# Kernel optimization log

Measured on AMD Instinct MI355X. Metric: run time of the kernel, lower is better.

Reference implementation:

```python
import jax, jax.numpy as jnp
import numpy as np

N = 100000      # num nodes (in_features)
E = 1600000     # num edges
P = 100000      # num pos/neg label edges
EMB = 64        # embedding dim (hardcoded 64 in Encoder)
HID = 128       # 2 * out_channels
OUT = 64        # out_channels
EPS = 1e-15     # PyG GAE EPS
MAX_LOGSTD = 10.0


def setup_inputs() -> dict:
    key = jax.random.key(0)
    ks = jax.random.split(key, 10)
    emb_weight = jax.random.normal(ks[0], (N, EMB), dtype=jnp.float32) * 0.1
    edge_index = jax.random.randint(ks[1], (2, E), 0, N, dtype=jnp.int64)
    pos_edge_label_index = jax.random.randint(ks[2], (2, P), 0, N, dtype=jnp.int64)
    neg_edge_label_index = jax.random.randint(ks[3], (2, P), 0, N, dtype=jnp.int64)
    W1 = jax.random.normal(ks[4], (EMB, HID), dtype=jnp.float32) / np.sqrt(EMB)
    b1 = jnp.zeros((HID,), dtype=jnp.float32)
    W_mu = jax.random.normal(ks[5], (HID, OUT), dtype=jnp.float32) / np.sqrt(HID)
    b_mu = jnp.zeros((OUT,), dtype=jnp.float32)
    W_ls = jax.random.normal(ks[6], (HID, OUT), dtype=jnp.float32) / np.sqrt(HID)
    b_ls = jnp.zeros((OUT,), dtype=jnp.float32)
    return {
        'emb_weight': emb_weight, 'edge_index': edge_index,
        'W1': W1, 'b1': b1, 'W_mu': W_mu, 'b_mu': b_mu, 'W_ls': W_ls, 'b_ls': b_ls,
        'pos_edge_label_index': pos_edge_label_index,
        'neg_edge_label_index': neg_edge_label_index,
    }


def gcn_conv(x, src, dst, deg_inv_sqrt, W, b):
    # GCNConv with added self-loops and symmetric normalization:
    # out = D^{-1/2} (A + I) D^{-1/2} (x W) + b
    h = x @ W                                  # [N, F_out]
    norm = deg_inv_sqrt[src] * deg_inv_sqrt[dst]          # [E]
    agg = jax.ops.segment_sum(h[src] * norm[:, None], dst, num_segments=N)
    agg = agg + h * (deg_inv_sqrt * deg_inv_sqrt)[:, None]  # self-loop term
    return agg + b


def reference(emb_weight, edge_index, W1, b1, W_mu, b_mu, W_ls, b_ls,
              pos_edge_label_index, neg_edge_label_index):
    src, dst = edge_index[0], edge_index[1]
    # degree includes self-loop weight 1
    deg = jax.ops.segment_sum(jnp.ones((E,), dtype=emb_weight.dtype), dst, num_segments=N) + 1.0
    deg_inv_sqrt = jax.lax.rsqrt(deg)

    h = jax.nn.relu(gcn_conv(emb_weight, src, dst, deg_inv_sqrt, W1, b1))
    mu = gcn_conv(h, src, dst, deg_inv_sqrt, W_mu, b_mu)
    logstd = jnp.minimum(gcn_conv(h, src, dst, deg_inv_sqrt, W_ls, b_ls), MAX_LOGSTD)
    z = mu  # eval-mode reparametrize returns mu

    # recon_loss: inner-product decoder + BCE on pos/neg label edges
    ps, pd = pos_edge_label_index[0], pos_edge_label_index[1]
    ns, nd = neg_edge_label_index[0], neg_edge_label_index[1]
    pos_p = jax.nn.sigmoid(jnp.sum(z[ps] * z[pd], axis=-1))
    neg_p = jax.nn.sigmoid(jnp.sum(z[ns] * z[nd], axis=-1))
    pos_loss = -jnp.mean(jnp.log(pos_p + EPS))
    neg_loss = -jnp.mean(jnp.log(1.0 - neg_p + EPS))
    loss = pos_loss + neg_loss
    return z, logstd, loss
```

## Files before the change

kernel.cpp:

```cpp
#include <hip/hip_runtime.h>
#include <hip/hip_bf16.h>
#include <hip/hip_fp16.h>

#define NN 100000
#define NE 1600000
#define NP 100000

typedef _Float16 h2v __attribute__((ext_vector_type(2)));

__device__ __forceinline__ float fdot2u(uint a, uint b, float c) {
    union { uint u; h2v h; } ua, ub;
    ua.u = a; ub.u = b;
    return __builtin_amdgcn_fdot2(ua.h, ub.h, c, false);
}

__device__ __forceinline__ uint packh2(float lo, float hi) {
    __half2 h = __floats2half2_rn(lo, hi);
    return *(uint*)&h;
}

__device__ __forceinline__ void h8_to_f(const uint4 u, float* f) {
    const __half2* hp = (const __half2*)&u;
    float2 t0 = __half22float2(hp[0]), t1 = __half22float2(hp[1]);
    float2 t2 = __half22float2(hp[2]), t3 = __half22float2(hp[3]);
    f[0] = t0.x; f[1] = t0.y; f[2] = t1.x; f[3] = t1.y;
    f[4] = t2.x; f[5] = t2.y; f[6] = t3.x; f[7] = t3.y;
}

__device__ __forceinline__ void add8(const uint4 u, float* acc) {
    float f[8]; h8_to_f(u, f);
#pragma unroll
    for (int i = 0; i < 8; ++i) acc[i] += f[i];
}

__device__ __forceinline__ uint4 f_to_h8(const float* f) {
    union { __half2 h[4]; uint4 u; } pk;
    pk.h[0] = __floats2half2_rn(f[0], f[1]);
    pk.h[1] = __floats2half2_rn(f[2], f[3]);
    pk.h[2] = __floats2half2_rn(f[4], f[5]);
    pk.h[3] = __floats2half2_rn(f[6], f[7]);
    return pk.u;
}

#define RNG 400
#define NBK 250
#define K_A 8000
#define CAPB 12288

__global__ __launch_bounds__(256) void k_hist(const int* __restrict__ ei,
                                              int* __restrict__ bcnt) {
    __shared__ int hist[NBK];
    int tid = threadIdx.x;
    int e0 = blockIdx.x * K_A;
    for (int i = tid; i < NBK; i += 256) hist[i] = 0;
    __syncthreads();
    for (int i = tid; i < K_A; i += 256) atomicAdd(&hist[ei[NE + e0 + i] / RNG], 1);
    __syncthreads();
    for (int i = tid; i < NBK; i += 256) if (hist[i]) atomicAdd(&bcnt[i], hist[i]);
}

__global__ __launch_bounds__(256) void k_bscan(const int* __restrict__ bcnt,
                                               int* __restrict__ bbase,
                                               int* __restrict__ gcnt) {
    __shared__ int c[NBK];
    int tid = threadIdx.x;
    if (tid < NBK) c[tid] = bcnt[tid];
    __syncthreads();
    if (tid < 64) {
        int run = 0;
        for (int g = 0; g < NBK; g += 64) {
            int idx = g + tid;
            int v = (idx < NBK) ? c[idx] : 0;
            int inc = v;
#pragma unroll
            for (int off = 1; off < 64; off <<= 1) {
                int t2 = __shfl_up(inc, off);
                if (tid >= off) inc += t2;
            }
            if (idx < NBK) { int ex = run + inc - v; bbase[idx] = ex; gcnt[idx] = ex; }
            run += __shfl(inc, 63);
        }
        if (tid == 0) bbase[NBK] = run;
    }
}

__global__ __launch_bounds__(256) void k_binA(const int* __restrict__ ei,
                                              int* __restrict__ gcnt,
                                              int* __restrict__ edges) {
    __shared__ int buf[K_A];
    __shared__ int hist[NBK], lofs[NBK + 1], lcnt[NBK], gbase[NBK];
    int tid = threadIdx.x;
    int e0 = blockIdx.x * K_A;
    for (int i = tid; i < NBK; i += 256) { hist[i] = 0; lcnt[i] = 0; }
    __syncthreads();
    for (int i = tid; i < K_A; i += 256) atomicAdd(&hist[ei[NE + e0 + i] / RNG], 1);
    __syncthreads();
    if (tid < 64) {
        int run = 0;
        for (int g = 0; g < NBK; g += 64) {
            int idx = g + tid;
            int v = (idx < NBK) ? hist[idx] : 0;
            int inc = v;
#pragma unroll
            for (int off = 1; off < 64; off <<= 1) {
                int t2 = __shfl_up(inc, off);
                if (tid >= off) inc += t2;
            }
            if (idx < NBK) lofs[idx] = run + inc - v;
            run += __shfl(inc, 63);
        }
        if (tid == 0) lofs[NBK] = run;
    }
    for (int i = tid; i < NBK; i += 256) gbase[i] = atomicAdd(&gcnt[i], hist[i]);
    __syncthreads();
    for (int i = tid; i < K_A; i += 256) {
        int s = ei[e0 + i], d = ei[NE + e0 + i];
        int b = d / RNG;
        int dl = d - b * RNG;
        int p = lofs[b] + atomicAdd(&lcnt[b], 1);
        buf[p] = s | (dl << 17);
    }
    __syncthreads();
    for (int j = tid; j < K_A; j += 256) {
        int loB = 0, hiB = NBK;
        while (hiB - loB > 1) {
            int mid = (loB + hiB) >> 1;
            if (lofs[mid] <= j) loB = mid; else hiB = mid;
        }
        edges[gbase[loB] + (j - lofs[loB])] = buf[j];
    }
}

__global__ __launch_bounds__(256) void k_binB(const int* __restrict__ bbase,
                                              int* __restrict__ edges,
                                              int* __restrict__ rowptr,
                                              float* __restrict__ dinv) {
    __shared__ int buf[CAPB];
    __shared__ int hist[RNG], lrp[RNG], lcnt[RNG];
    int tid = threadIdx.x;
    int b = blockIdx.x;
    int lo = b * RNG;
    int base = bbase[b], n = bbase[b + 1] - base;
    for (int i = tid; i < RNG; i += 256) { hist[i] = 0; lcnt[i] = 0; }
    __syncthreads();
    for (int i = tid; i < n; i += 256)
        atomicAdd(&hist[((unsigned)edges[base + i]) >> 17], 1);
    __syncthreads();
    if (tid < 64) {
        int run = 0;
        for (int g = 0; g < RNG; g += 64) {
            int idx = g + tid;
            int v = (idx < RNG) ? hist[idx] : 0;
            int inc = v;
#pragma unroll
            for (int off = 1; off < 64; off <<= 1) {
                int t2 = __shfl_up(inc, off);
                if (tid >= off) inc += t2;
            }
            if (idx < RNG) lrp[idx] = run + inc - v;
            run += __shfl(inc, 63);
        }
    }
    __syncthreads();
    for (int i = tid; i < RNG; i += 256) {
        dinv[lo + i] = rsqrtf((float)hist[i] + 1.0f);
        rowptr[lo + i] = base + lrp[i];
    }
    if (b == NBK - 1 && tid == 0) rowptr[NN] = base + n;
    int ovS0 = -1, ovS1 = -1, ovR0 = 0, ovR1 = 0;
    for (int i = tid; i < n; i += 256) {
        int rec = edges[base + i];
        int dl = ((unsigned)rec) >> 17;
        int src = rec & 0x1FFFF;
        int slot = lrp[dl] + atomicAdd(&lcnt[dl], 1);
        if (slot < CAPB) buf[slot] = src;
        else if (ovS0 < 0) { ovS0 = slot; ovR0 = src; }
        else { ovS1 = slot; ovR1 = src; }
    }
    __syncthreads();
    int lim = n < CAPB ? n : CAPB;
    for (int i = tid; i < lim; i += 256) edges[base + i] = buf[i];
    if (ovS0 >= 0) edges[base + ovS0] = ovR0;
    if (ovS1 >= 0) edges[base + ovS1] = ovR1;
}

__global__ void k_cvt(const float4* __restrict__ in4, const float* __restrict__ dinv,
                      uint4* __restrict__ out) {
    int t = blockIdx.x * blockDim.x + threadIdx.x;
    if (t >= NN * 8) return;
    float dv = dinv[t >> 3];
    float4 a = in4[t * 2], b = in4[t * 2 + 1];
    float f[8] = {a.x * dv, a.y * dv, a.z * dv, a.w * dv,
                  b.x * dv, b.y * dv, b.z * dv, b.w * dv};
    out[t] = f_to_h8(f);
}

__global__ __launch_bounds__(256) void k_aggE(const uint4* __restrict__ x16,
                                              const float* __restrict__ dinv,
                                              const int* __restrict__ rowptr,
                                              const int* __restrict__ edges,
                                              uint4* __restrict__ aggE16) {
    int t = blockIdx.x * blockDim.x + threadIdx.x;
    int r = t >> 3, q = t & 7;
    float dr = dinv[r];
    float acc[8];
    h8_to_f(x16[(size_t)r * 8 + q], acc);
    int j = rowptr[r], j1 = rowptr[r + 1];
    for (; j + 8 <= j1; j += 8) {
        int e[8]; uint4 v[8];
#pragma unroll
        for (int i = 0; i < 8; ++i) e[i] = edges[j + i];
#pragma unroll
        for (int i = 0; i < 8; ++i) v[i] = x16[(size_t)e[i] * 8 + q];
#pragma unroll
        for (int i = 0; i < 8; ++i) add8(v[i], acc);
    }
    if (j + 4 <= j1) {
        int e[4]; uint4 v[4];
#pragma unroll
        for (int i = 0; i < 4; ++i) e[i] = edges[j + i];
#pragma unroll
        for (int i = 0; i < 4; ++i) v[i] = x16[(size_t)e[i] * 8 + q];
#pragma unroll
        for (int i = 0; i < 4; ++i) add8(v[i], acc);
        j += 4;
    }
    for (; j < j1; ++j) add8(x16[(size_t)edges[j] * 8 + q], acc);
    float o[8];
#pragma unroll
    for (int i = 0; i < 8; ++i) o[i] = acc[i] * dr;
    aggE16[(size_t)r * 8 + q] = f_to_h8(o);
}

__global__ __launch_bounds__(256) void k_aggH(const uint4* __restrict__ x16,
                                              const float* __restrict__ dinv,
                                              const int* __restrict__ rowptr,
                                              const int* __restrict__ edges,
                                              uint4* __restrict__ aggH16) {
    int t = blockIdx.x * blockDim.x + threadIdx.x;
    int r = t >> 4, q = t & 15;
    float dr = dinv[r];
    float acc[8];
    h8_to_f(x16[(size_t)r * 16 + q], acc);
    int j = rowptr[r], j1 = rowptr[r + 1];
    for (; j + 8 <= j1; j += 8) {
        int e[8]; uint4 v[8];
#pragma unroll
        for (int i = 0; i < 8; ++i) e[i] = edges[j + i];
#pragma unroll
        for (int i = 0; i < 8; ++i) v[i] = x16[(size_t)e[i] * 16 + q];
#pragma unroll
        for (int i = 0; i < 8; ++i) add8(v[i], acc);
    }
    if (j + 4 <= j1) {
        int e[4]; uint4 v[4];
#pragma unroll
        for (int i = 0; i < 4; ++i) e[i] = edges[j + i];
#pragma unroll
        for (int i = 0; i < 4; ++i) v[i] = x16[(size_t)e[i] * 16 + q];
#pragma unroll
        for (int i = 0; i < 4; ++i) add8(v[i], acc);
        j += 4;
    }
    for (; j < j1; ++j) add8(x16[(size_t)edges[j] * 16 + q], acc);
    float o[8];
#pragma unroll
    for (int i = 0; i < 8; ++i) o[i] = acc[i] * dr;
    aggH16[(size_t)r * 16 + q] = f_to_h8(o);
}

__global__ __launch_bounds__(256) void k_h(const uint4* __restrict__ aggE16,
                                           const float4* __restrict__ W1_4,
                                           const float* __restrict__ b1,
                                           const float* __restrict__ dinv,
                                           uint2* __restrict__ h16) {
    __shared__ uint4 w16h[32 * 32];
    __shared__ uint rows16[32 * 32];
    __shared__ float sdinv[32];
    int t = threadIdx.x;
    int base = blockIdx.x * 32;
#pragma unroll
    for (int i = 0; i < 4; ++i) {
        int idx = t + i * 256;
        int kp = idx >> 5, jg = idx & 31;
        float4 we = W1_4[(2 * kp) * 32 + jg];
        float4 wo = W1_4[(2 * kp + 1) * 32 + jg];
        w16h[idx] = make_uint4(packh2(we.x, wo.x), packh2(we.y, wo.y),
                               packh2(we.z, wo.z), packh2(we.w, wo.w));
    }
    {
        int r = t >> 3, c = t & 7;
        ((uint4*)rows16)[r * 8 + c] = aggE16[(size_t)(base + r) * 8 + c];
    }
    if (t < 32) sdinv[t] = dinv[base + t];
    __syncthreads();
    int rg = t >> 5, jg = t & 31;
    int r0 = rg * 4;
    float4 bias = ((const float4*)b1)[jg];
    float acc[4][4];
#pragma unroll
    for (int r = 0; r < 4; ++r) {
        acc[r][0] = bias.x; acc[r][1] = bias.y; acc[r][2] = bias.z; acc[r][3] = bias.w;
    }
#pragma unroll 4
    for (int kp = 0; kp < 32; ++kp) {
        uint f0 = rows16[(r0 + 0) * 32 + kp];
        uint f1 = rows16[(r0 + 1) * 32 + kp];
        uint f2 = rows16[(r0 + 2) * 32 + kp];
        uint f3 = rows16[(r0 + 3) * 32 + kp];
        uint4 wv = w16h[kp * 32 + jg];
        acc[0][0] = fdot2u(f0, wv.x, acc[0][0]); acc[0][1] = fdot2u(f0, wv.y, acc[0][1]);
        acc[0][2] = fdot2u(f0, wv.z, acc[0][2]); acc[0][3] = fdot2u(f0, wv.w, acc[0][3]);
        acc[1][0] = fdot2u(f1, wv.x, acc[1][0]); acc[1][1] = fdot2u(f1, wv.y, acc[1][1]);
        acc[1][2] = fdot2u(f1, wv.z, acc[1][2]); acc[1][3] = fdot2u(f1, wv.w, acc[1][3]);
        acc[2][0] = fdot2u(f2, wv.x, acc[2][0]); acc[2][1] = fdot2u(f2, wv.y, acc[2][1]);
        acc[2][2] = fdot2u(f2, wv.z, acc[2][2]); acc[2][3] = fdot2u(f2, wv.w, acc[2][3]);
        acc[3][0] = fdot2u(f3, wv.x, acc[3][0]); acc[3][1] = fdot2u(f3, wv.y, acc[3][1]);
        acc[3][2] = fdot2u(f3, wv.z, acc[3][2]); acc[3][3] = fdot2u(f3, wv.w, acc[3][3]);
    }
#pragma unroll
    for (int r = 0; r < 4; ++r) {
        float dv = sdinv[r0 + r];
        union { __half2 h[2]; uint2 u; } pk;
        pk.h[0] = __floats2half2_rn(fmaxf(acc[r][0], 0.0f) * dv, fmaxf(acc[r][1], 0.0f) * dv);
        pk.h[1] = __floats2half2_rn(fmaxf(acc[r][2], 0.0f) * dv, fmaxf(acc[r][3], 0.0f) * dv);
        h16[(size_t)(base + r0 + r) * 32 + jg] = pk.u;
    }
}

__global__ __launch_bounds__(256) void k_out(const uint4* __restrict__ aggH16,
                                             const float4* __restrict__ Wmu4,
                                             const float* __restrict__ bmu,
                                             const float4* __restrict__ Wls4,
                                             const float* __restrict__ bls,
                                             float* __restrict__ out,
                                             uint2* __restrict__ z16) {
    __shared__ uint4 w16h[64 * 32];
    __shared__ uint rows16[32 * 64];
    int t = threadIdx.x;
    int base = blockIdx.x * 32;
#pragma unroll
    for (int i = 0; i < 8; ++i) {
        int idx = t + i * 256;
        int kp = idx >> 5, jg = idx & 31;
        int jj = (jg < 16) ? jg : (jg - 16);
        const float4* W = (jg < 16) ? Wmu4 : Wls4;
        float4 we = W[(2 * kp) * 16 + jj];
        float4 wo = W[(2 * kp + 1) * 16 + jj];
        w16h[idx] = make_uint4(packh2(we.x, wo.x), packh2(we.y, wo.y),
                               packh2(we.z, wo.z), packh2(we.w, wo.w));
    }
#pragma unroll
    for (int i = 0; i < 2; ++i) {
        int idx = t + i * 256;
        int r = idx >> 4, c = idx & 15;
        ((uint4*)rows16)[r * 16 + c] = aggH16[(size_t)(base + r) * 16 + c];
    }
    __syncthreads();
    int rg = t >> 5, jg = t & 31;
    int r0 = rg * 4;
    float4 bias = (jg < 16) ? ((const float4*)bmu)[jg] : ((const float4*)bls)[jg - 16];
    float acc[4][4];
#pragma unroll
    for (int r = 0; r < 4; ++r) {
        acc[r][0] = bias.x; acc[r][1] = bias.y; acc[r][2] = bias.z; acc[r][3] = bias.w;
    }
#pragma unroll 4
    for (int kp = 0; kp < 64; ++kp) {
        uint f0 = rows16[(r0 + 0) * 64 + kp];
        uint f1 = rows16[(r0 + 1) * 64 + kp];
        uint f2 = rows16[(r0 + 2) * 64 + kp];
        uint f3 = rows16[(r0 + 3) * 64 + kp];
        uint4 wv = w16h[kp * 32 + jg];
        acc[0][0] = fdot2u(f0, wv.x, acc[0][0]); acc[0][1] = fdot2u(f0, wv.y, acc[0][1]);
        acc[0][2] = fdot2u(f0, wv.z, acc[0][2]); acc[0][3] = fdot2u(f0, wv.w, acc[0][3]);
        acc[1][0] = fdot2u(f1, wv.x, acc[1][0]); acc[1][1] = fdot2u(f1, wv.y, acc[1][1]);
        acc[1][2] = fdot2u(f1, wv.z, acc[1][2]); acc[1][3] = fdot2u(f1, wv.w, acc[1][3]);
        acc[2][0] = fdot2u(f2, wv.x, acc[2][0]); acc[2][1] = fdot2u(f2, wv.y, acc[2][1]);
        acc[2][2] = fdot2u(f2, wv.z, acc[2][2]); acc[2][3] = fdot2u(f2, wv.w, acc[2][3]);
        acc[3][0] = fdot2u(f3, wv.x, acc[3][0]); acc[3][1] = fdot2u(f3, wv.y, acc[3][1]);
        acc[3][2] = fdot2u(f3, wv.z, acc[3][2]); acc[3][3] = fdot2u(f3, wv.w, acc[3][3]);
    }
    float4* out4 = (float4*)out;
    if (jg < 16) {
#pragma unroll
        for (int r = 0; r < 4; ++r) {
            out4[(size_t)(base + r0 + r) * 16 + jg] =
                make_float4(acc[r][0], acc[r][1], acc[r][2], acc[r][3]);
            union { __half2 h[2]; uint2 u; } pk;
            pk.h[0] = __floats2half2_rn(acc[r][0], acc[r][1]);
            pk.h[1] = __floats2half2_rn(acc[r][2], acc[r][3]);
            z16[(size_t)(base + r0 + r) * 16 + jg] = pk.u;
        }
    } else {
#pragma unroll
        for (int r = 0; r < 4; ++r) {
            float4 o = make_float4(fminf(acc[r][0], 10.0f), fminf(acc[r][1], 10.0f),
                                   fminf(acc[r][2], 10.0f), fminf(acc[r][3], 10.0f));
            out4[(size_t)NN * 16 + (size_t)(base + r0 + r) * 16 + (jg - 16)] = o;
        }
    }
}

__global__ __launch_bounds__(256) void k_loss(const int* __restrict__ pos,
                                              const int* __restrict__ neg,
                                              const uint2* __restrict__ z16,
                                              float* __restrict__ accum) {
    int t = blockIdx.x * blockDim.x + threadIdx.x;
    int grp = t >> 4, q = t & 15;
    int e0 = grp * 4;
    bool isNeg = e0 >= NP;
    const int* idx = isNeg ? neg : pos;
    int eb = isNeg ? e0 - NP : e0;
    int a0 = idx[eb + 0], b0 = idx[NP + eb + 0];
    int a1 = idx[eb + 1], b1 = idx[NP + eb + 1];
    int a2 = idx[eb + 2], b2 = idx[NP + eb + 2];
    int a3 = idx[eb + 3], b3 = idx[NP + eb + 3];
    uint2 ua0 = z16[(size_t)a0 * 16 + q], ub0 = z16[(size_t)b0 * 16 + q];
    uint2 ua1 = z16[(size_t)a1 * 16 + q], ub1 = z16[(size_t)b1 * 16 + q];
    uint2 ua2 = z16[(size_t)a2 * 16 + q], ub2 = z16[(size_t)b2 * 16 + q];
    uint2 ua3 = z16[(size_t)a3 * 16 + q], ub3 = z16[(size_t)b3 * 16 + q];
    float d0 = fdot2u(ua0.y, ub0.y, fdot2u(ua0.x, ub0.x, 0.0f));
    float d1 = fdot2u(ua1.y, ub1.y, fdot2u(ua1.x, ub1.x, 0.0f));
    float d2 = fdot2u(ua2.y, ub2.y, fdot2u(ua2.x, ub2.x, 0.0f));
    float d3 = fdot2u(ua3.y, ub3.y, fdot2u(ua3.x, ub3.x, 0.0f));
#pragma unroll
    for (int off = 1; off < 16; off <<= 1) {
        d0 += __shfl_xor(d0, off);
        d1 += __shfl_xor(d1, off);
        d2 += __shfl_xor(d2, off);
        d3 += __shfl_xor(d3, off);
    }
    __shared__ float bsum[2];
    if (threadIdx.x < 2) bsum[threadIdx.x] = 0.0f;
    __syncthreads();
    if (q == 0) {
        float term;
        if (isNeg) {
            term = logf(1.0f - 1.0f / (1.0f + expf(-d0)) + 1e-15f)
                 + logf(1.0f - 1.0f / (1.0f + expf(-d1)) + 1e-15f)
                 + logf(1.0f - 1.0f / (1.0f + expf(-d2)) + 1e-15f)
                 + logf(1.0f - 1.0f / (1.0f + expf(-d3)) + 1e-15f);
        } else {
            term = logf(1.0f / (1.0f + expf(-d0)) + 1e-15f)
                 + logf(1.0f / (1.0f + expf(-d1)) + 1e-15f)
                 + logf(1.0f / (1.0f + expf(-d2)) + 1e-15f)
                 + logf(1.0f / (1.0f + expf(-d3)) + 1e-15f);
        }
        atomicAdd(&bsum[isNeg ? 1 : 0], term);
    }
    __syncthreads();
    if (threadIdx.x < 2) atomicAdd(&accum[threadIdx.x], bsum[threadIdx.x]);
}

__global__ void k_fin(const float* __restrict__ accum, float* __restrict__ out) {
    out[(size_t)NN * 128] = -(accum[0] + accum[1]) * (1.0f / (float)NP);
}

extern "C" void kernel_launch(void* const* d_in, const int* in_sizes, int n_in,
                              void* d_out, int out_size, void* d_ws, size_t ws_size,
                              hipStream_t stream) {
    const float* emb = (const float*)d_in[0];
    const int*   ei  = (const int*)d_in[1];
    const float* W1  = (const float*)d_in[2];
    const float* b1  = (const float*)d_in[3];
    const float* Wmu = (const float*)d_in[4];
    const float* bmu = (const float*)d_in[5];
    const float* Wls = (const float*)d_in[6];
    const float* bls = (const float*)d_in[7];
    const int*   pos = (const int*)d_in[8];
    const int*   neg = (const int*)d_in[9];
    float* out = (float*)d_out;

    char* ws = (char*)d_ws;
    float* dinv   = (float*)(ws);
    int*   rowptr = (int*)  (ws + (512 << 10));
    int*   bcnt   = (int*)  (ws + (1024 << 10));
    int*   bbase  = (int*)  (ws + (1028 << 10));
    int*   gcnt   = (int*)  (ws + (1032 << 10));
    float* accum  = (float*)(ws + (1040 << 10));
    const size_t OFF_EDGES = (2048 << 10);
    const size_t OFF_H16   = OFF_EDGES + (size_t)NE * 4;
    const size_t OFF_E16   = OFF_H16 + (size_t)NN * 128 * 2;
    int*   edges  = (int*)(ws + OFF_EDGES);
    uint2* h16    = (uint2*)(ws + OFF_H16);
    uint2* z16    = (uint2*)(ws + OFF_H16);
    uint4* emb16  = (uint4*)(ws + OFF_E16);
    uint4* aggH16 = (uint4*)(ws + OFF_E16);
    uint4* aggE16 = (uint4*)out;

    hipMemsetAsync(bcnt, 0, NBK * sizeof(int), stream);
    hipMemsetAsync(accum, 0, 2 * sizeof(float), stream);

    k_hist <<<NE / K_A, 256, 0, stream>>>(ei, bcnt);
    k_bscan<<<1, 256, 0, stream>>>(bcnt, bbase, gcnt);
    k_binA <<<NE / K_A, 256, 0, stream>>>(ei, gcnt, edges);
    k_binB <<<NBK, 256, 0, stream>>>(bbase, edges, rowptr, dinv);

    k_cvt  <<<(NN * 8 + 255) / 256, 256, 0, stream>>>((const float4*)emb, dinv, emb16);

    k_aggE<<<(NN * 8) / 256, 256, 0, stream>>>(emb16, dinv, rowptr, edges, aggE16);
    k_h<<<NN / 32, 256, 0, stream>>>(aggE16, (const float4*)W1, b1, dinv, h16);

    k_aggH<<<(NN * 16) / 256, 256, 0, stream>>>((const uint4*)h16, dinv, rowptr, edges, aggH16);
    k_out<<<NN / 32, 256, 0, stream>>>(aggH16, (const float4*)Wmu, bmu,
                                       (const float4*)Wls, bls, out, z16);

    k_loss<<<(2 * NP * 16) / (256 * 4), 256, 0, stream>>>(pos, neg, z16, accum);
    k_fin<<<1, 1, 0, stream>>>(accum, out);
}
```

Baseline: 285.6 us.

## Fuse neighbor aggregation into the dense transform kernels for both GCN layers

Merges the gather-aggregate kernels with the following small matmul kernels, so each 64-row block aggregates neighbor features straight into shared memory and then applies the weights. This removes the global write and re-read of the intermediate aggregated fp16 buffers and drops two kernel launches. Blocks grow to 512 threads covering 64 rows, and layer two now has 8 threads per row, each handling 16 features with two loads per edge instead of one. The risk is lower occupancy from the larger shared-memory footprint and less memory-level parallelism in the irregular gather phase.

```diff
diff --git a/kernel.cpp b/kernel.cpp
--- a/kernel.cpp
+++ b/kernel.cpp
@@ -195,112 +195,69 @@
     out[t] = f_to_h8(f);
 }
 
-__global__ __launch_bounds__(256) void k_aggE(const uint4* __restrict__ x16,
-                                              const float* __restrict__ dinv,
-                                              const int* __restrict__ rowptr,
-                                              const int* __restrict__ edges,
-                                              uint4* __restrict__ aggE16) {
-    int t = blockIdx.x * blockDim.x + threadIdx.x;
-    int r = t >> 3, q = t & 7;
-    float dr = dinv[r];
-    float acc[8];
-    h8_to_f(x16[(size_t)r * 8 + q], acc);
-    int j = rowptr[r], j1 = rowptr[r + 1];
-    for (; j + 8 <= j1; j += 8) {
-        int e[8]; uint4 v[8];
-#pragma unroll
-        for (int i = 0; i < 8; ++i) e[i] = edges[j + i];
-#pragma unroll
-        for (int i = 0; i < 8; ++i) v[i] = x16[(size_t)e[i] * 8 + q];
-#pragma unroll
-        for (int i = 0; i < 8; ++i) add8(v[i], acc);
-    }
-    if (j + 4 <= j1) {
-        int e[4]; uint4 v[4];
-#pragma unroll
-        for (int i = 0; i < 4; ++i) e[i] = edges[j + i];
-#pragma unroll
-        for (int i = 0; i < 4; ++i) v[i] = x16[(size_t)e[i] * 8 + q];
-#pragma unroll
-        for (int i = 0; i < 4; ++i) add8(v[i], acc);
-        j += 4;
-    }
-    for (; j < j1; ++j) add8(x16[(size_t)edges[j] * 8 + q], acc);
-    float o[8];
-#pragma unroll
-    for (int i = 0; i < 8; ++i) o[i] = acc[i] * dr;
-    aggE16[(size_t)r * 8 + q] = f_to_h8(o);
-}
-
-__global__ __launch_bounds__(256) void k_aggH(const uint4* __restrict__ x16,
-                                              const float* __restrict__ dinv,
-                                              const int* __restrict__ rowptr,
-                                              const int* __restrict__ edges,
-                                              uint4* __restrict__ aggH16) {
-    int t = blockIdx.x * blockDim.x + threadIdx.x;
-    int r = t >> 4, q = t & 15;
-    float dr = dinv[r];
-    float acc[8];
-    h8_to_f(x16[(size_t)r * 16 + q], acc);
-    int j = rowptr[r], j1 = rowptr[r + 1];
-    for (; j + 8 <= j1; j += 8) {
-        int e[8]; uint4 v[8];
-#pragma unroll
-        for (int i = 0; i < 8; ++i) e[i] = edges[j + i];
-#pragma unroll
-        for (int i = 0; i < 8; ++i) v[i] = x16[(size_t)e[i] * 16 + q];
-#pragma unroll
-        for (int i = 0; i < 8; ++i) add8(v[i], acc);
-    }
-    if (j + 4 <= j1) {
-        int e[4]; uint4 v[4];
-#pragma unroll
-        for (int i = 0; i < 4; ++i) e[i] = edges[j + i];
-#pragma unroll
-        for (int i = 0; i < 4; ++i) v[i] = x16[(size_t)e[i] * 16 + q];
-#pragma unroll
-        for (int i = 0; i < 4; ++i) add8(v[i], acc);
-        j += 4;
-    }
-    for (; j < j1; ++j) add8(x16[(size_t)edges[j] * 16 + q], acc);
-    float o[8];
-#pragma unroll
-    for (int i = 0; i < 8; ++i) o[i] = acc[i] * dr;
-    aggH16[(size_t)r * 16 + q] = f_to_h8(o);
-}
-
-__global__ __launch_bounds__(256) void k_h(const uint4* __restrict__ aggE16,
-                                           const float4* __restrict__ W1_4,
-                                           const float* __restrict__ b1,
-                                           const float* __restrict__ dinv,
-                                           uint2* __restrict__ h16) {
+__global__ __launch_bounds__(512) void k_l1(const uint4* __restrict__ x16,
+                                            const float* __restrict__ dinv,
+                                            const int* __restrict__ rowptr,
+                                            const int* __restrict__ edges,
+                                            const float4* __restrict__ W1_4,
+                                            const float* __restrict__ b1,
+                                            uint2* __restrict__ h16) {
     __shared__ uint4 w16h[32 * 32];
-    __shared__ uint rows16[32 * 32];
-    __shared__ float sdinv[32];
+    __shared__ uint rows16[64 * 32];
+    __shared__ float sdinv[64];
     int t = threadIdx.x;
-    int base = blockIdx.x * 32;
-#pragma unroll
-    for (int i = 0; i < 4; ++i) {
-        int idx = t + i * 256;
+    int base = blockIdx.x * 64;
+#pragma unroll
+    for (int i = 0; i < 2; ++i) {
+        int idx = t + i * 512;
         int kp = idx >> 5, jg = idx & 31;
         float4 we = W1_4[(2 * kp) * 32 + jg];
         float4 wo = W1_4[(2 * kp + 1) * 32 + jg];
         w16h[idx] = make_uint4(packh2(we.x, wo.x), packh2(we.y, wo.y),
                                packh2(we.z, wo.z), packh2(we.w, wo.w));
     }
-    {
-        int r = t >> 3, c = t & 7;
-        ((uint4*)rows16)[r * 8 + c] = aggE16[(size_t)(base + r) * 8 + c];
-    }
-    if (t < 32) sdinv[t] = dinv[base + t];
+    if (t < 64) sdinv[t] = (base + t < NN) ? dinv[base + t] : 0.0f;
+    int rl = t >> 3, q = t & 7;
+    int r = base + rl;
+    if (r < NN) {
+        float acc[8];
+        h8_to_f(x16[(size_t)r * 8 + q], acc);
+        int j = rowptr[r], j1 = rowptr[r + 1];
+        for (; j + 8 <= j1; j += 8) {
+            int e[8]; uint4 v[8];
+#pragma unroll
+            for (int i = 0; i < 8; ++i) e[i] = edges[j + i];
+#pragma unroll
+            for (int i = 0; i < 8; ++i) v[i] = x16[(size_t)e[i] * 8 + q];
+#pragma unroll
+            for (int i = 0; i < 8; ++i) add8(v[i], acc);
+        }
+        if (j + 4 <= j1) {
+            int e[4]; uint4 v[4];
+#pragma unroll
+            for (int i = 0; i < 4; ++i) e[i] = edges[j + i];
+#pragma unroll
+            for (int i = 0; i < 4; ++i) v[i] = x16[(size_t)e[i] * 8 + q];
+#pragma unroll
+            for (int i = 0; i < 4; ++i) add8(v[i], acc);
+            j += 4;
+        }
+        for (; j < j1; ++j) add8(x16[(size_t)edges[j] * 8 + q], acc);
+        float dr = dinv[r];
+#pragma unroll
+        for (int i = 0; i < 8; ++i) acc[i] *= dr;
+#pragma unroll
+        for (int i = 0; i < 4; ++i)
+            rows16[rl * 32 + 4 * q + i] = packh2(acc[2 * i], acc[2 * i + 1]);
+    }
     __syncthreads();
     int rg = t >> 5, jg = t & 31;
     int r0 = rg * 4;
     float4 bias = ((const float4*)b1)[jg];
     float acc[4][4];
 #pragma unroll
-    for (int r = 0; r < 4; ++r) {
-        acc[r][0] = bias.x; acc[r][1] = bias.y; acc[r][2] = bias.z; acc[r][3] = bias.w;
+    for (int r2 = 0; r2 < 4; ++r2) {
+        acc[r2][0] = bias.x; acc[r2][1] = bias.y; acc[r2][2] = bias.z; acc[r2][3] = bias.w;
     }
 #pragma unroll 4
     for (int kp = 0; kp < 32; ++kp) {
@@ -319,29 +276,37 @@
         acc[3][2] = fdot2u(f3, wv.z, acc[3][2]); acc[3][3] = fdot2u(f3, wv.w, acc[3][3]);
     }
 #pragma unroll
-    for (int r = 0; r < 4; ++r) {
-        float dv = sdinv[r0 + r];
-        union { __half2 h[2]; uint2 u; } pk;
-        pk.h[0] = __floats2half2_rn(fmaxf(acc[r][0], 0.0f) * dv, fmaxf(acc[r][1], 0.0f) * dv);
-        pk.h[1] = __floats2half2_rn(fmaxf(acc[r][2], 0.0f) * dv, fmaxf(acc[r][3], 0.0f) * dv);
-        h16[(size_t)(base + r0 + r) * 32 + jg] = pk.u;
-    }
-}
-
-__global__ __launch_bounds__(256) void k_out(const uint4* __restrict__ aggH16,
-                                             const float4* __restrict__ Wmu4,
-                                             const float* __restrict__ bmu,
-                                             const float4* __restrict__ Wls4,
-                                             const float* __restrict__ bls,
-                                             float* __restrict__ out,
-                                             uint2* __restrict__ z16) {
+    for (int r2 = 0; r2 < 4; ++r2) {
+        int row = base + r0 + r2;
+        if (row < NN) {
+            float dv = sdinv[r0 + r2];
+            union { __half2 h[2]; uint2 u; } pk;
+            pk.h[0] = __floats2half2_rn(fmaxf(acc[r2][0], 0.0f) * dv,
+                                        fmaxf(acc[r2][1], 0.0f) * dv);
+            pk.h[1] = __floats2half2_rn(fmaxf(acc[r2][2], 0.0f) * dv,
+                                        fmaxf(acc[r2][3], 0.0f) * dv);
+            h16[(size_t)row * 32 + jg] = pk.u;
+        }
+    }
+}
+
+__global__ __launch_bounds__(512) void k_l2(const uint4* __restrict__ x16,
+                                            const float* __restrict__ dinv,
+                                            const int* __restrict__ rowptr,
+                                            const int* __restrict__ edges,
+                                            const float4* __restrict__ Wmu4,
+                                            const float* __restrict__ bmu,
+                                            const float4* __restrict__ Wls4,
+                                            const float* __restrict__ bls,
+                                            float* __restrict__ out,
+                                            uint2* __restrict__ z16) {
     __shared__ uint4 w16h[64 * 32];
-    __shared__ uint rows16[32 * 64];
+    __shared__ uint rows16[64 * 64];
     int t = threadIdx.x;
-    int base = blockIdx.x * 32;
-#pragma unroll
-    for (int i = 0; i < 8; ++i) {
-        int idx = t + i * 256;
+    int base = blockIdx.x * 64;
+#pragma unroll
+    for (int i = 0; i < 4; ++i) {
+        int idx = t + i * 512;
         int kp = idx >> 5, jg = idx & 31;
         int jj = (jg < 16) ? jg : (jg - 16);
         const float4* W = (jg < 16) ? Wmu4 : Wls4;
@@ -350,11 +315,39 @@
         w16h[idx] = make_uint4(packh2(we.x, wo.x), packh2(we.y, wo.y),
                                packh2(we.z, wo.z), packh2(we.w, wo.w));
     }
-#pragma unroll
-    for (int i = 0; i < 2; ++i) {
-        int idx = t + i * 256;
-        int r = idx >> 4, c = idx & 15;
-        ((uint4*)rows16)[r * 16 + c] = aggH16[(size_t)(base + r) * 16 + c];
+    int rl = t >> 3, q = t & 7;
+    int r = base + rl;
+    if (r < NN) {
+        float acc[16];
+        {
+            uint4 s0 = x16[(size_t)r * 16 + 2 * q];
+            uint4 s1 = x16[(size_t)r * 16 + 2 * q + 1];
+            h8_to_f(s0, acc); h8_to_f(s1, acc + 8);
+        }
+        int j = rowptr[r], j1 = rowptr[r + 1];
+        for (; j + 4 <= j1; j += 4) {
+            int e[4]; uint4 va[4], vb[4];
+#pragma unroll
+            for (int i = 0; i < 4; ++i) e[i] = edges[j + i];
+#pragma unroll
+            for (int i = 0; i < 4; ++i) {
+                va[i] = x16[(size_t)e[i] * 16 + 2 * q];
+                vb[i] = x16[(size_t)e[i] * 16 + 2 * q + 1];
+            }
+#pragma unroll
+            for (int i = 0; i < 4; ++i) { add8(va[i], acc); add8(vb[i], acc + 8); }
+        }
+        for (; j < j1; ++j) {
+            int e = edges[j];
+            add8(x16[(size_t)e * 16 + 2 * q], acc);
+            add8(x16[(size_t)e * 16 + 2 * q + 1], acc + 8);
+        }
+        float dr = dinv[r];
+#pragma unroll
+        for (int i = 0; i < 16; ++i) acc[i] *= dr;
+#pragma unroll
+        for (int i = 0; i < 8; ++i)
+            rows16[rl * 64 + 8 * q + i] = packh2(acc[2 * i], acc[2 * i + 1]);
     }
     __syncthreads();
     int rg = t >> 5, jg = t & 31;
@@ -362,8 +355,8 @@
     float4 bias = (jg < 16) ? ((const float4*)bmu)[jg] : ((const float4*)bls)[jg - 16];
     float acc[4][4];
 #pragma unroll
-    for (int r = 0; r < 4; ++r) {
-        acc[r][0] = bias.x; acc[r][1] = bias.y; acc[r][2] = bias.z; acc[r][3] = bias.w;
+    for (int r2 = 0; r2 < 4; ++r2) {
+        acc[r2][0] = bias.x; acc[r2][1] = bias.y; acc[r2][2] = bias.z; acc[r2][3] = bias.w;
     }
 #pragma unroll 4
     for (int kp = 0; kp < 64; ++kp) {
@@ -384,20 +377,26 @@
     float4* out4 = (float4*)out;
     if (jg < 16) {
 #pragma unroll
-        for (int r = 0; r < 4; ++r) {
-            out4[(size_t)(base + r0 + r) * 16 + jg] =
-                make_float4(acc[r][0], acc[r][1], acc[r][2], acc[r][3]);
-            union { __half2 h[2]; uint2 u; } pk;
-            pk.h[0] = __floats2half2_rn(acc[r][0], acc[r][1]);
-            pk.h[1] = __floats2half2_rn(acc[r][2], acc[r][3]);
-            z16[(size_t)(base + r0 + r) * 16 + jg] = pk.u;
+        for (int r2 = 0; r2 < 4; ++r2) {
+            int row = base + r0 + r2;
+            if (row < NN) {
+                out4[(size_t)row * 16 + jg] =
+                    make_float4(acc[r2][0], acc[r2][1], acc[r2][2], acc[r2][3]);
+                union { __half2 h[2]; uint2 u; } pk;
+                pk.h[0] = __floats2half2_rn(acc[r2][0], acc[r2][1]);
+                pk.h[1] = __floats2half2_rn(acc[r2][2], acc[r2][3]);
+                z16[(size_t)row * 16 + jg] = pk.u;
+            }
         }
     } else {
 #pragma unroll
-        for (int r = 0; r < 4; ++r) {
-            float4 o = make_float4(fminf(acc[r][0], 10.0f), fminf(acc[r][1], 10.0f),
-                                   fminf(acc[r][2], 10.0f), fminf(acc[r][3], 10.0f));
-            out4[(size_t)NN * 16 + (size_t)(base + r0 + r) * 16 + (jg - 16)] = o;
+        for (int r2 = 0; r2 < 4; ++r2) {
+            int row = base + r0 + r2;
+            if (row < NN) {
+                float4 o = make_float4(fminf(acc[r2][0], 10.0f), fminf(acc[r2][1], 10.0f),
+                                       fminf(acc[r2][2], 10.0f), fminf(acc[r2][3], 10.0f));
+                out4[(size_t)NN * 16 + (size_t)row * 16 + (jg - 16)] = o;
+            }
         }
     }
 }
@@ -484,10 +483,8 @@
     const size_t OFF_E16   = OFF_H16 + (size_t)NN * 128 * 2;
     int*   edges  = (int*)(ws + OFF_EDGES);
     uint2* h16    = (uint2*)(ws + OFF_H16);
-    uint2* z16    = (uint2*)(ws + OFF_H16);
     uint4* emb16  = (uint4*)(ws + OFF_E16);
-    uint4* aggH16 = (uint4*)(ws + OFF_E16);
-    uint4* aggE16 = (uint4*)out;
+    uint2* z16    = (uint2*)(ws + OFF_E16);
 
     hipMemsetAsync(bcnt, 0, NBK * sizeof(int), stream);
     hipMemsetAsync(accum, 0, 2 * sizeof(float), stream);
@@ -499,12 +496,12 @@
 
     k_cvt  <<<(NN * 8 + 255) / 256, 256, 0, stream>>>((const float4*)emb, dinv, emb16);
 
-    k_aggE<<<(NN * 8) / 256, 256, 0, stream>>>(emb16, dinv, rowptr, edges, aggE16);
-    k_h<<<NN / 32, 256, 0, stream>>>(aggE16, (const float4*)W1, b1, dinv, h16);
-
-    k_aggH<<<(NN * 16) / 256, 256, 0, stream>>>((const uint4*)h16, dinv, rowptr, edges, aggH16);
-    k_out<<<NN / 32, 256, 0, stream>>>(aggH16, (const float4*)Wmu, bmu,
-                                       (const float4*)Wls, bls, out, z16);
+    const int GB = (NN + 63) / 64;
+    k_l1<<<GB, 512, 0, stream>>>(emb16, dinv, rowptr, edges,
+                                 (const float4*)W1, b1, h16);
+    k_l2<<<GB, 512, 0, stream>>>((const uint4*)h16, dinv, rowptr, edges,
+                                 (const float4*)Wmu, bmu, (const float4*)Wls, bls,
+                                 out, z16);
 
     k_loss<<<(2 * NP * 16) / (256 * 4), 256, 0, stream>>>(pos, neg, z16, accum);
     k_fin<<<1, 1, 0, stream>>>(accum, out);
```

Result: no change. 282.4 us (-1.1%).
